# Optimization experiments

Measured on AMD Instinct MI355X. Metric: run time of the kernel, lower is better.

Reference implementation:

```python
import jax, jax.numpy as jnp
import numpy as np

N = 100000      # nodes
E = 1600000     # edges (avg degree 16)
IN = 64         # input feature dim
HID = 64        # hidden dim per head
HEADS = 4
OUT = 7         # hardcoded out_dim in GCNNet


def setup_inputs() -> dict:
    key = jax.random.key(0)
    ks = jax.random.split(key, 24)

    def p(k, shape, fan_in):
        return jax.random.normal(k, shape, jnp.float32) / jnp.float32(np.sqrt(fan_in))

    inp = {}
    inp["feature"] = jax.random.normal(ks[0], (N, IN), jnp.float32)
    inp["src"] = jax.random.randint(ks[1], (E,), 0, N, jnp.int32)
    inp["dst"] = jax.random.randint(ks[2], (E,), 0, N, jnp.int32)
    # layer 0: 4 heads (IN->HID) + head_linear GCN_Attention (4*HID->HID)
    inp["W0"] = p(ks[3], (HEADS, IN, HID), IN)
    inp["b0"] = jnp.zeros((HEADS, HID), jnp.float32)
    inp["a0"] = p(ks[4], (HEADS, 2 * HID), 2 * HID)
    inp["W0h"] = p(ks[5], (HEADS * HID, HID), HEADS * HID)
    inp["b0h"] = jnp.zeros((HID,), jnp.float32)
    inp["a0h"] = p(ks[6], (2 * HID,), 2 * HID)
    # layer 1: 4 heads (HID->HID) + head_linear (4*HID->HID)
    inp["W1"] = p(ks[7], (HEADS, HID, HID), HID)
    inp["b1"] = jnp.zeros((HEADS, HID), jnp.float32)
    inp["a1"] = p(ks[8], (HEADS, 2 * HID), 2 * HID)
    inp["W1h"] = p(ks[9], (HEADS * HID, HID), HEADS * HID)
    inp["b1h"] = jnp.zeros((HID,), jnp.float32)
    inp["a1h"] = p(ks[10], (2 * HID,), 2 * HID)
    # out layer: mean mode, 4 heads (HID->OUT) + Linear(OUT, OUT)
    inp["Wo"] = p(ks[11], (HEADS, HID, OUT), HID)
    inp["bo"] = jnp.zeros((HEADS, OUT), jnp.float32)
    inp["ao"] = p(ks[12], (HEADS, 2 * OUT), 2 * OUT)
    inp["lin_W"] = p(ks[13], (OUT, OUT), OUT)   # stored (in, out)
    inp["lin_b"] = jnp.zeros((OUT,), jnp.float32)
    return inp


def gcn_attn(feat, W, b, a, src, dst):
    """One GCN_Attention layer: edge score = GELU(attn_fc(cat(z_src, z_dst))),
    per-dst softmax over incoming edges, weighted sum of src z."""
    z = feat @ W + b                       # [N, d]
    d = z.shape[1]
    # attn_fc has no bias: attn(cat(s, t)) = s @ a[:d] + t @ a[d:]
    s_l = z @ a[:d]                        # [N]
    s_r = z @ a[d:]                        # [N]
    e = jax.nn.gelu(s_l[src] + s_r[dst], approximate=False)   # [E]
    # segmented softmax over incoming edges of each dst node
    m = jax.ops.segment_max(e, dst, num_segments=N)
    m = jnp.where(jnp.isfinite(m), m, 0.0)
    ex = jnp.exp(e - m[dst])
    denom = jax.ops.segment_sum(ex, dst, num_segments=N)
    alpha = ex / denom[dst]                # [E]
    h = jax.ops.segment_sum(alpha[:, None] * z[src], dst, num_segments=N)  # [N, d]
    return h


def reference(feature, src, dst, W0, b0, a0, W0h, b0h, a0h,
              W1, b1, a1, W1h, b1h, a1h, Wo, bo, ao, lin_W, lin_b):
    # layer 0 (concat mode)
    h0 = jnp.concatenate([gcn_attn(feature, W0[i], b0[i], a0[i], src, dst)
                          for i in range(HEADS)], axis=1)      # [N, 4*HID]
    f1 = gcn_attn(h0, W0h, b0h, a0h, src, dst)                 # [N, HID]
    # layer 1 (concat mode)
    h1 = jnp.concatenate([gcn_attn(f1, W1[i], b1[i], a1[i], src, dst)
                          for i in range(HEADS)], axis=1)
    f2 = gcn_attn(h1, W1h, b1h, a1h, src, dst)                 # [N, HID]
    # out layer (mean mode)
    outs = jnp.mean(jnp.stack([gcn_attn(f2, Wo[i], bo[i], ao[i], src, dst)
                               for i in range(HEADS)]), axis=0)  # [N, OUT]
    out = outs @ lin_W + lin_b
    return jax.nn.softmax(out, axis=1)
```

## Files before the change

### kernel.cpp

```cpp
#include <hip/hip_runtime.h>
#include <hip/hip_bf16.h>
#include <math.h>

#define HEADS 4
#define HID 64
#define OUTD 7

typedef __attribute__((ext_vector_type(8))) short bf16x8;
typedef __attribute__((ext_vector_type(4))) float f32x4;

__device__ __forceinline__ float gelu_exact(float x) {
    return 0.5f * x * (1.0f + erff(x * 0.70710678118654752f));
}

__device__ __forceinline__ float readlane_f(float v, int k) {
    union { float f; int i; } u;
    u.f = v;
    u.i = __builtin_amdgcn_readlane(u.i, k);
    return u.f;
}
__device__ __forceinline__ int readlane_i(int v, int k) {
    return __builtin_amdgcn_readlane(v, k);
}

__device__ __forceinline__ unsigned int f2bf(float f) {
    unsigned int x = __float_as_uint(f);
    return (x + 0x7fffu + ((x >> 16) & 1u)) >> 16;
}
__device__ __forceinline__ float bf_lo(unsigned int v) {
    return __uint_as_float(v << 16);
}
__device__ __forceinline__ float bf_hi(unsigned int v) {
    return __uint_as_float(v & 0xffff0000u);
}


__global__ void hist_kernel(const int* __restrict__ dst, int* __restrict__ cnt, int E) {
    for (int e = blockIdx.x * blockDim.x + threadIdx.x; e < E; e += gridDim.x * blockDim.x)
        atomicAdd(&cnt[dst[e]], 1);
}

__global__ __launch_bounds__(256) void scan1_kernel(const int* __restrict__ cnt,
                                                    int* __restrict__ rowptr,
                                                    int* __restrict__ bsum, int Nn) {
    __shared__ int sums[256];
    int t = threadIdx.x;
    int base = blockIdx.x * 2048 + t * 8;
    int orig[8];
    int run = 0;
#pragma unroll
    for (int i = 0; i < 8; i++) {
        orig[i] = (base + i < Nn) ? cnt[base + i] : 0;
        run += orig[i];
    }
    sums[t] = run;
    __syncthreads();
    for (int off = 1; off < 256; off <<= 1) {
        int y = (t >= off) ? sums[t - off] : 0;
        __syncthreads();
        sums[t] += y;
        __syncthreads();
    }
    int excl = sums[t] - run;
    if (t == 255) bsum[blockIdx.x] = sums[255];
    int e = excl;
#pragma unroll
    for (int i = 0; i < 8; i++) {
        if (base + i < Nn) rowptr[base + i] = e;
        e += orig[i];
    }
}

__global__ void scan2_kernel(int* __restrict__ bsum, int* __restrict__ rowptr, int nb, int Nn) {
    if (blockIdx.x == 0 && threadIdx.x == 0) {
        int run = 0;
        for (int i = 0; i < nb; i++) {
            int t = bsum[i];
            bsum[i] = run;
            run += t;
        }
        rowptr[Nn] = run;
    }
}

__global__ void scan3_kernel(int* __restrict__ rowptr, const int* __restrict__ bsum, int Nn) {
    int i = blockIdx.x * blockDim.x + threadIdx.x;
    if (i < Nn) rowptr[i] += bsum[i >> 11];
}

__global__ void scatter_kernel(const int* __restrict__ dst, const int* __restrict__ rowptr,
                               int* __restrict__ cnt, const int* __restrict__ srcv,
                               int* __restrict__ srcp, int E) {
    for (int e = blockIdx.x * blockDim.x + threadIdx.x; e < E; e += gridDim.x * blockDim.x) {
        int d = dst[e];
        int p = rowptr[d] + atomicAdd(&cnt[d], 1);
        srcp[p] = srcv[e];
    }
}

__global__ void wconv_kernel(const float* __restrict__ W, unsigned short* __restrict__ Wt) {
    int m = blockIdx.x, k = threadIdx.x;
    Wt[m * 256 + k] = (unsigned short)f2bf(W[k * 64 + m]);
}


template <int MODE>
__global__ __launch_bounds__(256, 2) void gemm_kernel(const float* __restrict__ X,
                                                      const float* __restrict__ Wt,
                                                      const float* __restrict__ Bt,
                                                      const float* __restrict__ Aw,
                                                      unsigned short* __restrict__ Zb,
                                                      float* __restrict__ Zf,
                                                      float* __restrict__ SLo,
                                                      float* __restrict__ SRo, int Nn) {
    constexpr int K = 64;
    constexpr int M = (MODE == 0) ? 256 : 32;
    constexpr int CPL = (MODE == 0) ? 4 : 1;

    __shared__ float wlds[K * M];

    const int tid = threadIdx.x;
    const int wid = tid >> 6;
    const int lane = tid & 63;
    const int row0 = blockIdx.x * 32 + wid * 8;

    if (MODE == 0) {
#pragma unroll
        for (int it = 0; it < 16; ++it) {
            int flat = it * 1024 + tid * 4;
            int k = flat >> 8, m = flat & 255;
            int h = m >> 6, c = m & 63;
            *(float4*)&wlds[flat] = *(const float4*)(Wt + h * 4096 + k * 64 + c);
        }
    } else {
#pragma unroll
        for (int it = 0; it < 8; ++it) {
            int idx = it * 256 + tid;
            int k = idx >> 5, m = idx & 31, h = m >> 3, j = m & 7;
            wlds[idx] = (j < 7) ? Wt[h * 448 + k * 7 + j] : 0.f;
        }
    }
    __syncthreads();

    float acc[8][CPL];
#pragma unroll
    for (int r = 0; r < 8; ++r)
#pragma unroll
        for (int c = 0; c < CPL; ++c) acc[r][c] = 0.f;

    float xr[8];
#pragma unroll
    for (int r = 0; r < 8; ++r) {
        int rr = row0 + r;
        rr = (rr < Nn) ? rr : (Nn - 1);
        xr[r] = X[(size_t)rr * 64 + lane];
    }
#pragma unroll 4
    for (int k = 0; k < 64; ++k) {
        if (MODE == 0) {
            float4 wv = *(const float4*)&wlds[k * 256 + lane * 4];
#pragma unroll
            for (int r = 0; r < 8; ++r) {
                float xk = readlane_f(xr[r], k);
                acc[r][0] = fmaf(xk, wv.x, acc[r][0]);
                acc[r][1] = fmaf(xk, wv.y, acc[r][1]);
                acc[r][2] = fmaf(xk, wv.z, acc[r][2]);
                acc[r][3] = fmaf(xk, wv.w, acc[r][3]);
            }
        } else {
            float wv = wlds[k * 32 + (lane & 31)];
#pragma unroll
            for (int r = 0; r < 8; ++r)
                acc[r][0] = fmaf(readlane_f(xr[r], k), wv, acc[r][0]);
        }
    }

    if (MODE == 0) {
        float4 bv = *(const float4*)(Bt + lane * 4);
        const int h = lane >> 4;
        const int c0 = (lane & 15) * 4;
        float4 al4 = *(const float4*)(Aw + h * 128 + c0);
        float4 ar4 = *(const float4*)(Aw + h * 128 + 64 + c0);
        const int t = lane;
        const int lsbase = t >> 2;
#pragma unroll
        for (int r = 0; r < 8; ++r) {
            int row = row0 + r;
            float4 s = {acc[r][0] + bv.x, acc[r][1] + bv.y, acc[r][2] + bv.z, acc[r][3] + bv.w};
            float sp = s.x * al4.x + s.y * al4.y + s.z * al4.z + s.w * al4.w;
            float rp = s.x * ar4.x + s.y * ar4.y + s.z * ar4.z + s.w * ar4.w;
#pragma unroll
            for (int o = 1; o < 16; o <<= 1) {
                sp += __shfl_xor(sp, o);
                rp += __shfl_xor(rp, o);
            }
            unsigned int lo = f2bf(s.x) | (f2bf(s.y) << 16);
            unsigned int hi = f2bf(s.z) | (f2bf(s.w) << 16);
            unsigned int us[4];
#pragma unroll
            for (int h2 = 0; h2 < 4; ++h2) {
                int ls = (h2 << 4) | lsbase;
                unsigned int vlo = (unsigned int)__shfl((int)lo, ls);
                unsigned int vhi = (unsigned int)__shfl((int)hi, ls);
                unsigned int v = (t & 2) ? vhi : vlo;
                us[h2] = (t & 1) ? (v >> 16) : (v & 0xffffu);
            }
            if (row < Nn) {
                uint2 pk = {us[0] | (us[1] << 16), us[2] | (us[3] << 16)};
                *(uint2*)(Zb + (size_t)row * 256 + t * 4) = pk;
                if ((lane & 15) == 0) {
                    SLo[(size_t)row * 4 + h] = sp;
                    SRo[(size_t)row * 4 + h] = rp;
                }
            }
        }
    } else {
        if (lane < 32) {
            int m = lane, h = m >> 3, j = m & 7;
            float bvv = (j < 7) ? Bt[h * 7 + j] : 0.f;
            float al = (j < 7) ? Aw[h * 14 + j] : 0.f;
            float ar = (j < 7) ? Aw[h * 14 + 7 + j] : 0.f;
#pragma unroll
            for (int r = 0; r < 8; ++r) {
                int row = row0 + r;
                float zv = (j < 7) ? acc[r][0] + bvv : 0.f;
                float sp = zv * al, rp = zv * ar;
#pragma unroll
                for (int o = 1; o < 8; o <<= 1) {
                    sp += __shfl_xor(sp, o);
                    rp += __shfl_xor(rp, o);
                }
                if (row < Nn) {
                    Zf[(size_t)row * 32 + m] = zv;
                    if (j == 0) {
                        SLo[(size_t)row * 4 + h] = sp;
                        SRo[(size_t)row * 4 + h] = rp;
                    }
                }
            }
        }
    }
}


__global__ __launch_bounds__(256) void gemm1_mfma_kernel(
    const unsigned short* __restrict__ X, const unsigned short* __restrict__ Wt,
    const float* __restrict__ Bt, const float* __restrict__ Aw,
    unsigned short* __restrict__ Zb, float* __restrict__ SLo, float* __restrict__ SRo,
    int Nn) {
    const int tid = threadIdx.x;
    const int wid = tid >> 6;
    const int lane = tid & 63;
    const int g = lane >> 4, i = lane & 15;
    const int rowbase = blockIdx.x * 64 + wid * 16;

    int arow = rowbase + i;
    if (arow >= Nn) arow = Nn - 1;
    const bf16x8* xa = (const bf16x8*)(X + (size_t)arow * 256 + g * 8);
    const bf16x8* w0 = (const bf16x8*)(Wt + (size_t)(i) * 256 + g * 8);
    const bf16x8* w1 = (const bf16x8*)(Wt + (size_t)(16 + i) * 256 + g * 8);
    const bf16x8* w2 = (const bf16x8*)(Wt + (size_t)(32 + i) * 256 + g * 8);
    const bf16x8* w3 = (const bf16x8*)(Wt + (size_t)(48 + i) * 256 + g * 8);

    f32x4 acc0 = {0.f, 0.f, 0.f, 0.f};
    f32x4 acc1 = acc0, acc2 = acc0, acc3 = acc0;
#pragma unroll
    for (int ks = 0; ks < 8; ++ks) {
        bf16x8 av = xa[ks * 4];
        bf16x8 b0 = w0[ks * 4];
        bf16x8 b1 = w1[ks * 4];
        bf16x8 b2 = w2[ks * 4];
        bf16x8 b3 = w3[ks * 4];
        acc0 = __builtin_amdgcn_mfma_f32_16x16x32_bf16(av, b0, acc0, 0, 0, 0);
        acc1 = __builtin_amdgcn_mfma_f32_16x16x32_bf16(av, b1, acc1, 0, 0, 0);
        acc2 = __builtin_amdgcn_mfma_f32_16x16x32_bf16(av, b2, acc2, 0, 0, 0);
        acc3 = __builtin_amdgcn_mfma_f32_16x16x32_bf16(av, b3, acc3, 0, 0, 0);
    }

    float bv0 = Bt[i], bv1 = Bt[16 + i], bv2 = Bt[32 + i], bv3 = Bt[48 + i];
    float al0 = Aw[i], al1 = Aw[16 + i], al2 = Aw[32 + i], al3 = Aw[48 + i];
    float ar0 = Aw[64 + i], ar1 = Aw[80 + i], ar2 = Aw[96 + i], ar3 = Aw[112 + i];
    float z0[4], z1[4], z2[4], z3[4], sp[4], rp[4];
#pragma unroll
    for (int r = 0; r < 4; ++r) {
        z0[r] = acc0[r] + bv0;
        z1[r] = acc1[r] + bv1;
        z2[r] = acc2[r] + bv2;
        z3[r] = acc3[r] + bv3;
        sp[r] = z0[r] * al0 + z1[r] * al1 + z2[r] * al2 + z3[r] * al3;
        rp[r] = z0[r] * ar0 + z1[r] * ar1 + z2[r] * ar2 + z3[r] * ar3;
    }
#pragma unroll
    for (int o = 1; o <= 8; o <<= 1) {
#pragma unroll
        for (int r = 0; r < 4; ++r) {
            sp[r] += __shfl_xor(sp[r], o);
            rp[r] += __shfl_xor(rp[r], o);
        }
    }
#pragma unroll
    for (int r = 0; r < 4; ++r) {
        int row = rowbase + g * 4 + r;
        if (row < Nn) {
            unsigned short* zp = Zb + (size_t)row * 64 + i;
            zp[0] = (unsigned short)f2bf(z0[r]);
            zp[16] = (unsigned short)f2bf(z1[r]);
            zp[32] = (unsigned short)f2bf(z2[r]);
            zp[48] = (unsigned short)f2bf(z3[r]);
            if (i == 0) {
                SLo[row] = sp[r];
                SRo[row] = rp[r];
            }
        }
    }
}


#define MAX4_REDUCE(m0, m1, m2, m3)                      \
    _Pragma("unroll") for (int off = 32; off; off >>= 1) { \
        m0 = fmaxf(m0, __shfl_xor(m0, off));             \
        m1 = fmaxf(m1, __shfl_xor(m1, off));             \
        m2 = fmaxf(m2, __shfl_xor(m2, off));             \
        m3 = fmaxf(m3, __shfl_xor(m3, off));             \
    }

#define SUM4_REDUCE(d0, d1, d2, d3)                      \
    _Pragma("unroll") for (int off = 32; off; off >>= 1) { \
        d0 += __shfl_xor(d0, off);                       \
        d1 += __shfl_xor(d1, off);                       \
        d2 += __shfl_xor(d2, off);                       \
        d3 += __shfl_xor(d3, off);                       \
    }

__global__ __launch_bounds__(256) void aggregate4_kernel(
    const unsigned short* __restrict__ Zb, const float* __restrict__ SL,
    const float* __restrict__ SR, const int* __restrict__ rowptr,
    const int* __restrict__ srcp, unsigned short* __restrict__ Hb, int Nn) {
    __shared__ int sstage[4][64];
    __shared__ float4 wstage[4][64];
    int wid = threadIdx.x >> 6;
    int n = (blockIdx.x * blockDim.x + threadIdx.x) >> 6;
    int lane = threadIdx.x & 63;
    if (n >= Nn) return;
    int s0 = rowptr[n], s1 = rowptr[n + 1];
    int deg = s1 - s0;
    unsigned short* hp = Hb + (size_t)n * 256 + lane;
    if (deg == 0) {
        hp[0] = 0; hp[64] = 0; hp[128] = 0; hp[192] = 0;
        return;
    }
    const float4 sr4 = *(const float4*)(SR + (size_t)n * 4);
    float hx = 0.f, hy = 0.f, hz = 0.f, hw = 0.f;
    float d0 = 0.f, d1 = 0.f, d2 = 0.f, d3 = 0.f;
    const unsigned laneoff = (unsigned)(lane * 8);

#define AGG4_EDGE_LDS(JJ)                                                    \
    {                                                                        \
        int s = sstage[wid][(JJ)];                                           \
        float4 w = wstage[wid][(JJ)];                                        \
        uint2 q = *(const uint2*)((const char*)Zb + ((unsigned)s * 512u + laneoff)); \
        hx = fmaf(w.x, bf_lo(q.x), hx);                                      \
        hy = fmaf(w.y, bf_hi(q.x), hy);                                      \
        hz = fmaf(w.z, bf_lo(q.y), hz);                                      \
        hw = fmaf(w.w, bf_hi(q.y), hw);                                      \
    }

    if (deg <= 64) {
        float e0 = -INFINITY, e1 = -INFINITY, e2 = -INFINITY, e3 = -INFINITY;
        int sv = 0;
        if (lane < deg) {
            sv = srcp[s0 + lane];
            float4 sl4 = *(const float4*)(SL + (size_t)sv * 4);
            e0 = gelu_exact(sl4.x + sr4.x);
            e1 = gelu_exact(sl4.y + sr4.y);
            e2 = gelu_exact(sl4.z + sr4.z);
            e3 = gelu_exact(sl4.w + sr4.w);
        }
        float m0 = e0, m1 = e1, m2 = e2, m3 = e3;
        MAX4_REDUCE(m0, m1, m2, m3)
        float ex0 = 0.f, ex1 = 0.f, ex2 = 0.f, ex3 = 0.f;
        if (lane < deg) {
            ex0 = __expf(e0 - m0); ex1 = __expf(e1 - m1);
            ex2 = __expf(e2 - m2); ex3 = __expf(e3 - m3);
        }
        d0 = ex0; d1 = ex1; d2 = ex2; d3 = ex3;
        if (lane < deg) {
            sstage[wid][lane] = sv;
            wstage[wid][lane] = make_float4(ex0, ex1, ex2, ex3);
        }
        int jj = 0;
        for (; jj + 3 < deg; jj += 4) {
            AGG4_EDGE_LDS(jj)
            AGG4_EDGE_LDS(jj + 1)
            AGG4_EDGE_LDS(jj + 2)
            AGG4_EDGE_LDS(jj + 3)
        }
        for (; jj < deg; ++jj) AGG4_EDGE_LDS(jj)
    } else {
        float m0 = -INFINITY, m1 = -INFINITY, m2 = -INFINITY, m3 = -INFINITY;
        for (int base = s0; base < s1; base += 64) {
            int j = base + lane;
            if (j < s1) {
                int s = srcp[j];
                float4 sl4 = *(const float4*)(SL + (size_t)s * 4);
                m0 = fmaxf(m0, gelu_exact(sl4.x + sr4.x));
                m1 = fmaxf(m1, gelu_exact(sl4.y + sr4.y));
                m2 = fmaxf(m2, gelu_exact(sl4.z + sr4.z));
                m3 = fmaxf(m3, gelu_exact(sl4.w + sr4.w));
            }
        }
        MAX4_REDUCE(m0, m1, m2, m3)
        for (int base = s0; base < s1; base += 64) {
            int j = base + lane;
            int sv = 0;
            float ex0 = 0.f, ex1 = 0.f, ex2 = 0.f, ex3 = 0.f;
            if (j < s1) {
                sv = srcp[j];
                float4 sl4 = *(const float4*)(SL + (size_t)sv * 4);
                ex0 = __expf(gelu_exact(sl4.x + sr4.x) - m0);
                ex1 = __expf(gelu_exact(sl4.y + sr4.y) - m1);
                ex2 = __expf(gelu_exact(sl4.z + sr4.z) - m2);
                ex3 = __expf(gelu_exact(sl4.w + sr4.w) - m3);
            }
            d0 += ex0; d1 += ex1; d2 += ex2; d3 += ex3;
            int cs = min(64, s1 - base);
            for (int jj = 0; jj < cs; ++jj) {
                int s = readlane_i(sv, jj);
                float a0 = readlane_f(ex0, jj), a1 = readlane_f(ex1, jj);
                float a2 = readlane_f(ex2, jj), a3 = readlane_f(ex3, jj);
                uint2 q = *(const uint2*)((const char*)Zb + ((unsigned)s * 512u + laneoff));
                hx = fmaf(a0, bf_lo(q.x), hx);
                hy = fmaf(a1, bf_hi(q.x), hy);
                hz = fmaf(a2, bf_lo(q.y), hz);
                hw = fmaf(a3, bf_hi(q.y), hw);
            }
        }
    }
#undef AGG4_EDGE_LDS
    SUM4_REDUCE(d0, d1, d2, d3)
    hp[0] = (unsigned short)f2bf(hx / d0);
    hp[64] = (unsigned short)f2bf(hy / d1);
    hp[128] = (unsigned short)f2bf(hz / d2);
    hp[192] = (unsigned short)f2bf(hw / d3);
}

__global__ __launch_bounds__(256) void aggregate1_kernel(
    const unsigned short* __restrict__ Zb, const float* __restrict__ SL,
    const float* __restrict__ SR, const int* __restrict__ rowptr,
    const int* __restrict__ srcp, float* __restrict__ Hout, int Nn) {
    __shared__ int s1s[4][64];
    __shared__ float w1s[4][64];
    int wid = threadIdx.x >> 6;
    int n = (blockIdx.x * blockDim.x + threadIdx.x) >> 6;
    int lane = threadIdx.x & 63;
    if (n >= Nn) return;
    int s0 = rowptr[n], s1 = rowptr[n + 1];
    int deg = s1 - s0;
    if (deg == 0) {
        Hout[(size_t)n * 64 + lane] = 0.f;
        return;
    }
    const float srn = SR[n];
    float hacc = 0.f, den = 0.f;
    const unsigned laneoff = (unsigned)(lane * 2);

    if (deg <= 64) {
        float e = -INFINITY;
        int sv = 0;
        if (lane < deg) {
            sv = srcp[s0 + lane];
            e = gelu_exact(SL[sv] + srn);
        }
        float m = e;
#pragma unroll
        for (int off = 32; off; off >>= 1) m = fmaxf(m, __shfl_xor(m, off));
        float ex = (lane < deg) ? __expf(e - m) : 0.f;
        den = ex;
        if (lane < deg) {
            s1s[wid][lane] = sv;
            w1s[wid][lane] = ex;
        }
        int jj = 0;
        for (; jj + 3 < deg; jj += 4) {
#pragma unroll
            for (int u = 0; u < 4; ++u) {
                int s = s1s[wid][jj + u];
                float b = w1s[wid][jj + u];
                unsigned short zq = *(const unsigned short*)((const char*)Zb +
                                                             ((unsigned)s * 128u + laneoff));
                hacc = fmaf(b, bf_lo((unsigned int)zq), hacc);
            }
        }
        for (; jj < deg; ++jj) {
            int s = s1s[wid][jj];
            float b = w1s[wid][jj];
            unsigned short zq = *(const unsigned short*)((const char*)Zb +
                                                         ((unsigned)s * 128u + laneoff));
            hacc = fmaf(b, bf_lo((unsigned int)zq), hacc);
        }
    } else {
        float m = -INFINITY;
        for (int base = s0; base < s1; base += 64) {
            int j = base + lane;
            if (j < s1) m = fmaxf(m, gelu_exact(SL[srcp[j]] + srn));
        }
#pragma unroll
        for (int off = 32; off; off >>= 1) m = fmaxf(m, __shfl_xor(m, off));
        for (int base = s0; base < s1; base += 64) {
            int j = base + lane;
            int sv = 0;
            float ex = 0.f;
            if (j < s1) {
                sv = srcp[j];
                ex = __expf(gelu_exact(SL[sv] + srn) - m);
            }
            den += ex;
            int cs = min(64, s1 - base);
            for (int jj = 0; jj < cs; ++jj) {
                int s = readlane_i(sv, jj);
                float b = readlane_f(ex, jj);
                hacc = fmaf(b, bf_lo((unsigned int)Zb[(size_t)s * 64 + lane]), hacc);
            }
        }
    }
#pragma unroll
    for (int off = 32; off; off >>= 1) den += __shfl_xor(den, off);
    Hout[(size_t)n * 64 + lane] = hacc / den;
}

__global__ __launch_bounds__(256) void aggregateo_kernel(
    const float* __restrict__ Z, const float* __restrict__ SL, const float* __restrict__ SR,
    const int* __restrict__ rowptr, const int* __restrict__ srcp,
    float* __restrict__ Hout, int Nn) {
    int n = (blockIdx.x * blockDim.x + threadIdx.x) >> 6;
    int lane = threadIdx.x & 63;
    if (n >= Nn) return;
    int s0 = rowptr[n], s1 = rowptr[n + 1];
    int deg = s1 - s0;
    if (deg == 0) {
        if (lane < 32) Hout[(size_t)n * 32 + lane] = 0.f;
        return;
    }
    const float4 sr4 = *(const float4*)(SR + (size_t)n * 4);
    const int h = (lane & 31) >> 3;
    const int eo = lane >> 5;
    float hacc = 0.f;
    float d0 = 0.f, d1 = 0.f, d2 = 0.f, d3 = 0.f;
    const float* zl = Z + (lane & 31);

    if (deg <= 64) {
        float e0 = -INFINITY, e1 = -INFINITY, e2 = -INFINITY, e3 = -INFINITY;
        int sv = 0;
        if (lane < deg) {
            sv = srcp[s0 + lane];
            float4 sl4 = *(const float4*)(SL + (size_t)sv * 4);
            e0 = gelu_exact(sl4.x + sr4.x);
            e1 = gelu_exact(sl4.y + sr4.y);
            e2 = gelu_exact(sl4.z + sr4.z);
            e3 = gelu_exact(sl4.w + sr4.w);
        }
        float m0 = e0, m1 = e1, m2 = e2, m3 = e3;
        MAX4_REDUCE(m0, m1, m2, m3)
        float ex0 = 0.f, ex1 = 0.f, ex2 = 0.f, ex3 = 0.f;
        if (lane < deg) {
            ex0 = __expf(e0 - m0); ex1 = __expf(e1 - m1);
            ex2 = __expf(e2 - m2); ex3 = __expf(e3 - m3);
        }
        d0 = ex0; d1 = ex1; d2 = ex2; d3 = ex3;
        for (int jj = 0; jj < deg; jj += 2) {
            int lsrc = jj + eo;
            int s = __shfl(sv, lsrc);
            float b0 = __shfl(ex0, lsrc), b1 = __shfl(ex1, lsrc);
            float b2 = __shfl(ex2, lsrc), b3 = __shfl(ex3, lsrc);
            float exs = (h == 0) ? b0 : (h == 1) ? b1 : (h == 2) ? b2 : b3;
            hacc = fmaf(exs, zl[(size_t)s * 32], hacc);
        }
    } else {
        float m0 = -INFINITY, m1 = -INFINITY, m2 = -INFINITY, m3 = -INFINITY;
        for (int base = s0; base < s1; base += 64) {
            int j = base + lane;
            if (j < s1) {
                int s = srcp[j];
                float4 sl4 = *(const float4*)(SL + (size_t)s * 4);
                m0 = fmaxf(m0, gelu_exact(sl4.x + sr4.x));
                m1 = fmaxf(m1, gelu_exact(sl4.y + sr4.y));
                m2 = fmaxf(m2, gelu_exact(sl4.z + sr4.z));
                m3 = fmaxf(m3, gelu_exact(sl4.w + sr4.w));
            }
        }
        MAX4_REDUCE(m0, m1, m2, m3)
        for (int base = s0; base < s1; base += 64) {
            int j = base + lane;
            int sv = 0;
            float ex0 = 0.f, ex1 = 0.f, ex2 = 0.f, ex3 = 0.f;
            if (j < s1) {
                sv = srcp[j];
                float4 sl4 = *(const float4*)(SL + (size_t)sv * 4);
                ex0 = __expf(gelu_exact(sl4.x + sr4.x) - m0);
                ex1 = __expf(gelu_exact(sl4.y + sr4.y) - m1);
                ex2 = __expf(gelu_exact(sl4.z + sr4.z) - m2);
                ex3 = __expf(gelu_exact(sl4.w + sr4.w) - m3);
            }
            d0 += ex0; d1 += ex1; d2 += ex2; d3 += ex3;
            int cs = min(64, s1 - base);
            for (int jj = 0; jj < cs; jj += 2) {
                int lsrc = jj + eo;
                int s = __shfl(sv, lsrc);
                float b0 = __shfl(ex0, lsrc), b1 = __shfl(ex1, lsrc);
                float b2 = __shfl(ex2, lsrc), b3 = __shfl(ex3, lsrc);
                float exs = (h == 0) ? b0 : (h == 1) ? b1 : (h == 2) ? b2 : b3;
                hacc = fmaf(exs, zl[(size_t)s * 32], hacc);
            }
        }
    }
    SUM4_REDUCE(d0, d1, d2, d3)
    hacc += __shfl_xor(hacc, 32);
    float dsel = (h == 0) ? d0 : (h == 1) ? d1 : (h == 2) ? d2 : d3;
    if (lane < 32) Hout[(size_t)n * 32 + lane] = hacc / dsel;
}


__global__ void finalize_kernel(const float* __restrict__ Hs, const float* __restrict__ LW,
                                const float* __restrict__ LB, float* __restrict__ out, int Nn) {
    int n = blockIdx.x * blockDim.x + threadIdx.x;
    if (n >= Nn) return;
    float mean[7];
#pragma unroll
    for (int k = 0; k < 7; k++)
        mean[k] = 0.25f * (Hs[(size_t)n * 32 + k] + Hs[(size_t)n * 32 + 8 + k] +
                           Hs[(size_t)n * 32 + 16 + k] + Hs[(size_t)n * 32 + 24 + k]);
    float lg[7];
#pragma unroll
    for (int o = 0; o < 7; o++) {
        float acc = LB[o];
#pragma unroll
        for (int k = 0; k < 7; k++) acc = fmaf(mean[k], LW[k * 7 + o], acc);
        lg[o] = acc;
    }
    float mx = lg[0];
#pragma unroll
    for (int o = 1; o < 7; o++) mx = fmaxf(mx, lg[o]);
    float s = 0.f;
#pragma unroll
    for (int o = 0; o < 7; o++) {
        lg[o] = __expf(lg[o] - mx);
        s += lg[o];
    }
    float inv = 1.f / s;
#pragma unroll
    for (int o = 0; o < 7; o++) out[(size_t)n * 7 + o] = lg[o] * inv;
}


extern "C" void kernel_launch(void* const* d_in, const int* in_sizes, int n_in,
                              void* d_out, int out_size, void* d_ws, size_t ws_size,
                              hipStream_t stream) {
    const float* feature = (const float*)d_in[0];
    const int* src = (const int*)d_in[1];
    const int* dst = (const int*)d_in[2];
    const float* W0 = (const float*)d_in[3];
    const float* b0 = (const float*)d_in[4];
    const float* a0 = (const float*)d_in[5];
    const float* W0h = (const float*)d_in[6];
    const float* b0h = (const float*)d_in[7];
    const float* a0h = (const float*)d_in[8];
    const float* W1 = (const float*)d_in[9];
    const float* b1 = (const float*)d_in[10];
    const float* a1 = (const float*)d_in[11];
    const float* W1h = (const float*)d_in[12];
    const float* b1h = (const float*)d_in[13];
    const float* a1h = (const float*)d_in[14];
    const float* Wo = (const float*)d_in[15];
    const float* bo = (const float*)d_in[16];
    const float* ao = (const float*)d_in[17];
    const float* linW = (const float*)d_in[18];
    const float* linb = (const float*)d_in[19];
    const int N = in_sizes[0] / 64;
    const int E = in_sizes[1];
    float* out = (float*)d_out;

    char* ws = (char*)d_ws;
    size_t off = 0;
    auto alloc = [&](size_t bytes) {
        void* p = ws + off;
        off += (bytes + 255) & ~(size_t)255;
        return p;
    };
    int* cnt = (int*)alloc((size_t)N * 4);
    int* rowptr = (int*)alloc(((size_t)N + 1) * 4);
    int* bsum = (int*)alloc(256 * 4);
    int* srcp = (int*)alloc((size_t)E * 4);
    unsigned short* zbf = (unsigned short*)alloc((size_t)N * 256 * 2);
    unsigned short* hbufb = (unsigned short*)alloc((size_t)N * 256 * 2);
    unsigned short* wtb = (unsigned short*)alloc(64 * 256 * 2);
    float* zo = (float*)alloc((size_t)N * 32 * 4);
    float* fbuf = (float*)alloc((size_t)N * 64 * 4);
    float* slb = (float*)alloc((size_t)N * 4 * 4);
    float* srb = (float*)alloc((size_t)N * 4 * 4);
    float* houts = fbuf;

    hipMemsetAsync(cnt, 0, (size_t)N * 4, stream);
    hist_kernel<<<2048, 256, 0, stream>>>(dst, cnt, E);
    int nb = (N + 2047) / 2048;
    scan1_kernel<<<nb, 256, 0, stream>>>(cnt, rowptr, bsum, N);
    scan2_kernel<<<1, 32, 0, stream>>>(bsum, rowptr, nb, N);
    scan3_kernel<<<(N + 255) / 256, 256, 0, stream>>>(rowptr, bsum, N);
    hipMemsetAsync(cnt, 0, (size_t)N * 4, stream);
    scatter_kernel<<<2048, 256, 0, stream>>>(dst, rowptr, cnt, src, srcp, E);

    int gemm_blocks = (N + 31) / 32;
    int mfma_blocks = (N + 63) / 64;
    int ablk = (N + 3) / 4;

    gemm_kernel<0><<<gemm_blocks, 256, 0, stream>>>(feature, W0, b0, a0, zbf, nullptr, slb, srb, N);
    aggregate4_kernel<<<ablk, 256, 0, stream>>>(zbf, slb, srb, rowptr, srcp, hbufb, N);
    wconv_kernel<<<64, 256, 0, stream>>>(W0h, wtb);
    gemm1_mfma_kernel<<<mfma_blocks, 256, 0, stream>>>(hbufb, wtb, b0h, a0h, zbf, slb, srb, N);
    aggregate1_kernel<<<ablk, 256, 0, stream>>>(zbf, slb, srb, rowptr, srcp, fbuf, N);
    gemm_kernel<0><<<gemm_blocks, 256, 0, stream>>>(fbuf, W1, b1, a1, zbf, nullptr, slb, srb, N);
    aggregate4_kernel<<<ablk, 256, 0, stream>>>(zbf, slb, srb, rowptr, srcp, hbufb, N);
    wconv_kernel<<<64, 256, 0, stream>>>(W1h, wtb);
    gemm1_mfma_kernel<<<mfma_blocks, 256, 0, stream>>>(hbufb, wtb, b1h, a1h, zbf, slb, srb, N);
    aggregate1_kernel<<<ablk, 256, 0, stream>>>(zbf, slb, srb, rowptr, srcp, fbuf, N);
    gemm_kernel<2><<<gemm_blocks, 256, 0, stream>>>(fbuf, Wo, bo, ao, nullptr, zo, slb, srb, N);
    aggregateo_kernel<<<ablk, 256, 0, stream>>>(zo, slb, srb, rowptr, srcp, houts, N);
    finalize_kernel<<<(N + 255) / 256, 256, 0, stream>>>(houts, linW, linb, out, N);
}
```

Measured before the change: 1.025 ms.

## Use bf16 MFMA for head projections, store hidden features as bf16, record scatter ranks

Replaces the scalar readlane-based FP32 GEMM for the 4-head projections with a bf16 MFMA kernel. This needs a feature-to-bf16 conversion kernel and a transposed bf16 weight conversion. aggregate1 now writes its output in bf16, which feeds both the next MFMA GEMM and the output-layer GEMM, halving that buffer's traffic. The CSR build records per-edge atomic ranks during the histogram so the scatter pass needs no second atomic pass or memset. The cost is extra bf16 rounding of inputs and intermediate features, plus an extra rank array of size E.

Result: faster. 900.9 us (-12.1%).

```diff
diff --git a/kernel.cpp b/kernel.cpp
--- a/kernel.cpp
+++ b/kernel.cpp
@@ -34,10 +34,10 @@
     return __uint_as_float(v & 0xffff0000u);
 }
 
-
-__global__ void hist_kernel(const int* __restrict__ dst, int* __restrict__ cnt, int E) {
+__global__ void histrank_kernel(const int* __restrict__ dst, int* __restrict__ cnt,
+                                int* __restrict__ rank, int E) {
     for (int e = blockIdx.x * blockDim.x + threadIdx.x; e < E; e += gridDim.x * blockDim.x)
-        atomicAdd(&cnt[dst[e]], 1);
+        rank[e] = atomicAdd(&cnt[dst[e]], 1);
 }
 
 __global__ __launch_bounds__(256) void scan1_kernel(const int* __restrict__ cnt,
@@ -88,155 +88,108 @@
     if (i < Nn) rowptr[i] += bsum[i >> 11];
 }
 
-__global__ void scatter_kernel(const int* __restrict__ dst, const int* __restrict__ rowptr,
-                               int* __restrict__ cnt, const int* __restrict__ srcv,
-                               int* __restrict__ srcp, int E) {
-    for (int e = blockIdx.x * blockDim.x + threadIdx.x; e < E; e += gridDim.x * blockDim.x) {
-        int d = dst[e];
-        int p = rowptr[d] + atomicAdd(&cnt[d], 1);
-        srcp[p] = srcv[e];
-    }
-}
-
-__global__ void wconv_kernel(const float* __restrict__ W, unsigned short* __restrict__ Wt) {
+__global__ void scatter2_kernel(const int* __restrict__ dst, const int* __restrict__ rank,
+                                const int* __restrict__ rowptr, const int* __restrict__ srcv,
+                                int* __restrict__ srcp, int E) {
+    for (int e = blockIdx.x * blockDim.x + threadIdx.x; e < E; e += gridDim.x * blockDim.x)
+        srcp[rowptr[dst[e]] + rank[e]] = srcv[e];
+}
+
+__global__ void xconv_kernel(const float* __restrict__ X, unsigned short* __restrict__ Xb,
+                             int total4) {
+    int idx = blockIdx.x * blockDim.x + threadIdx.x;
+    if (idx < total4) {
+        float4 v = ((const float4*)X)[idx];
+        ushort4 o = {(unsigned short)f2bf(v.x), (unsigned short)f2bf(v.y),
+                     (unsigned short)f2bf(v.z), (unsigned short)f2bf(v.w)};
+        ((ushort4*)Xb)[idx] = o;
+    }
+}
+
+__global__ void wconv1_kernel(const float* __restrict__ W, unsigned short* __restrict__ Wt) {
     int m = blockIdx.x, k = threadIdx.x;
     Wt[m * 256 + k] = (unsigned short)f2bf(W[k * 64 + m]);
 }
 
-
-template <int MODE>
-__global__ __launch_bounds__(256, 2) void gemm_kernel(const float* __restrict__ X,
-                                                      const float* __restrict__ Wt,
-                                                      const float* __restrict__ Bt,
-                                                      const float* __restrict__ Aw,
-                                                      unsigned short* __restrict__ Zb,
-                                                      float* __restrict__ Zf,
-                                                      float* __restrict__ SLo,
-                                                      float* __restrict__ SRo, int Nn) {
-    constexpr int K = 64;
-    constexpr int M = (MODE == 0) ? 256 : 32;
-    constexpr int CPL = (MODE == 0) ? 4 : 1;
-
-    __shared__ float wlds[K * M];
-
-    const int tid = threadIdx.x;
-    const int wid = tid >> 6;
-    const int lane = tid & 63;
-    const int row0 = blockIdx.x * 32 + wid * 8;
-
-    if (MODE == 0) {
-#pragma unroll
-        for (int it = 0; it < 16; ++it) {
-            int flat = it * 1024 + tid * 4;
-            int k = flat >> 8, m = flat & 255;
-            int h = m >> 6, c = m & 63;
-            *(float4*)&wlds[flat] = *(const float4*)(Wt + h * 4096 + k * 64 + c);
-        }
-    } else {
-#pragma unroll
-        for (int it = 0; it < 8; ++it) {
-            int idx = it * 256 + tid;
-            int k = idx >> 5, m = idx & 31, h = m >> 3, j = m & 7;
-            wlds[idx] = (j < 7) ? Wt[h * 448 + k * 7 + j] : 0.f;
-        }
-    }
-    __syncthreads();
-
-    float acc[8][CPL];
-#pragma unroll
-    for (int r = 0; r < 8; ++r)
-#pragma unroll
-        for (int c = 0; c < CPL; ++c) acc[r][c] = 0.f;
-
-    float xr[8];
-#pragma unroll
-    for (int r = 0; r < 8; ++r) {
-        int rr = row0 + r;
-        rr = (rr < Nn) ? rr : (Nn - 1);
-        xr[r] = X[(size_t)rr * 64 + lane];
-    }
-#pragma unroll 4
-    for (int k = 0; k < 64; ++k) {
-        if (MODE == 0) {
-            float4 wv = *(const float4*)&wlds[k * 256 + lane * 4];
-#pragma unroll
-            for (int r = 0; r < 8; ++r) {
-                float xk = readlane_f(xr[r], k);
-                acc[r][0] = fmaf(xk, wv.x, acc[r][0]);
-                acc[r][1] = fmaf(xk, wv.y, acc[r][1]);
-                acc[r][2] = fmaf(xk, wv.z, acc[r][2]);
-                acc[r][3] = fmaf(xk, wv.w, acc[r][3]);
-            }
-        } else {
-            float wv = wlds[k * 32 + (lane & 31)];
-#pragma unroll
-            for (int r = 0; r < 8; ++r)
-                acc[r][0] = fmaf(readlane_f(xr[r], k), wv, acc[r][0]);
-        }
-    }
-
-    if (MODE == 0) {
-        float4 bv = *(const float4*)(Bt + lane * 4);
-        const int h = lane >> 4;
-        const int c0 = (lane & 15) * 4;
-        float4 al4 = *(const float4*)(Aw + h * 128 + c0);
-        float4 ar4 = *(const float4*)(Aw + h * 128 + 64 + c0);
-        const int t = lane;
-        const int lsbase = t >> 2;
-#pragma unroll
-        for (int r = 0; r < 8; ++r) {
-            int row = row0 + r;
-            float4 s = {acc[r][0] + bv.x, acc[r][1] + bv.y, acc[r][2] + bv.z, acc[r][3] + bv.w};
-            float sp = s.x * al4.x + s.y * al4.y + s.z * al4.z + s.w * al4.w;
-            float rp = s.x * ar4.x + s.y * ar4.y + s.z * ar4.z + s.w * ar4.w;
-#pragma unroll
-            for (int o = 1; o < 16; o <<= 1) {
-                sp += __shfl_xor(sp, o);
-                rp += __shfl_xor(rp, o);
-            }
-            unsigned int lo = f2bf(s.x) | (f2bf(s.y) << 16);
-            unsigned int hi = f2bf(s.z) | (f2bf(s.w) << 16);
-            unsigned int us[4];
-#pragma unroll
-            for (int h2 = 0; h2 < 4; ++h2) {
-                int ls = (h2 << 4) | lsbase;
-                unsigned int vlo = (unsigned int)__shfl((int)lo, ls);
-                unsigned int vhi = (unsigned int)__shfl((int)hi, ls);
-                unsigned int v = (t & 2) ? vhi : vlo;
-                us[h2] = (t & 1) ? (v >> 16) : (v & 0xffffu);
-            }
-            if (row < Nn) {
-                uint2 pk = {us[0] | (us[1] << 16), us[2] | (us[3] << 16)};
-                *(uint2*)(Zb + (size_t)row * 256 + t * 4) = pk;
-                if ((lane & 15) == 0) {
-                    SLo[(size_t)row * 4 + h] = sp;
-                    SRo[(size_t)row * 4 + h] = rp;
-                }
-            }
-        }
-    } else {
-        if (lane < 32) {
-            int m = lane, h = m >> 3, j = m & 7;
-            float bvv = (j < 7) ? Bt[h * 7 + j] : 0.f;
-            float al = (j < 7) ? Aw[h * 14 + j] : 0.f;
-            float ar = (j < 7) ? Aw[h * 14 + 7 + j] : 0.f;
-#pragma unroll
-            for (int r = 0; r < 8; ++r) {
-                int row = row0 + r;
-                float zv = (j < 7) ? acc[r][0] + bvv : 0.f;
-                float sp = zv * al, rp = zv * ar;
-#pragma unroll
-                for (int o = 1; o < 8; o <<= 1) {
-                    sp += __shfl_xor(sp, o);
-                    rp += __shfl_xor(rp, o);
-                }
-                if (row < Nn) {
-                    Zf[(size_t)row * 32 + m] = zv;
-                    if (j == 0) {
-                        SLo[(size_t)row * 4 + h] = sp;
-                        SRo[(size_t)row * 4 + h] = rp;
-                    }
-                }
+__global__ void wconv0_kernel(const float* __restrict__ W, unsigned short* __restrict__ Wt) {
+    int m = blockIdx.x, k = threadIdx.x;
+    int h = m >> 6, c = m & 63;
+    Wt[m * 64 + k] = (unsigned short)f2bf(W[h * 4096 + k * 64 + c]);
+}
+
+
+__global__ __launch_bounds__(256) void gemm0_mfma_kernel(
+    const unsigned short* __restrict__ Xb, const unsigned short* __restrict__ Wt,
+    const float* __restrict__ Bt, const float* __restrict__ Aw,
+    unsigned short* __restrict__ Zb, float* __restrict__ SLo, float* __restrict__ SRo,
+    int Nn) {
+    const int wid = threadIdx.x >> 6;
+    const int lane = threadIdx.x & 63;
+    const int g = lane >> 4, i = lane & 15;
+    const int rowbase = blockIdx.x * 64 + wid * 16;
+    int arow = rowbase + i;
+    if (arow >= Nn) arow = Nn - 1;
+    const bf16x8* xa = (const bf16x8*)(Xb + (size_t)arow * 64 + g * 8);
+
+    f32x4 acc[16];
+#pragma unroll
+    for (int j = 0; j < 16; ++j) acc[j] = (f32x4){0.f, 0.f, 0.f, 0.f};
+#pragma unroll
+    for (int ks = 0; ks < 2; ++ks) {
+        bf16x8 av = xa[ks * 4];
+#pragma unroll
+        for (int j = 0; j < 16; ++j) {
+            bf16x8 bv = *(const bf16x8*)(Wt + (size_t)(16 * j + i) * 64 + ks * 32 + g * 8);
+            acc[j] = __builtin_amdgcn_mfma_f32_16x16x32_bf16(av, bv, acc[j], 0, 0, 0);
+        }
+    }
+    float bvv[4][4], alv[4][4], arv[4][4];
+#pragma unroll
+    for (int h = 0; h < 4; ++h)
+#pragma unroll
+        for (int jj = 0; jj < 4; ++jj) {
+            int c = 16 * jj + i;
+            bvv[h][jj] = Bt[64 * h + c];
+            alv[h][jj] = Aw[h * 128 + c];
+            arv[h][jj] = Aw[h * 128 + 64 + c];
+        }
+#pragma unroll
+    for (int r = 0; r < 4; ++r) {
+        int row = rowbase + g * 4 + r;
+        float z[4][4], sp[4], rp[4];
+#pragma unroll
+        for (int h = 0; h < 4; ++h) {
+            sp[h] = 0.f;
+            rp[h] = 0.f;
+        }
+#pragma unroll
+        for (int h = 0; h < 4; ++h)
+#pragma unroll
+            for (int jj = 0; jj < 4; ++jj) {
+                float zv = acc[4 * h + jj][r] + bvv[h][jj];
+                z[h][jj] = zv;
+                sp[h] = fmaf(zv, alv[h][jj], sp[h]);
+                rp[h] = fmaf(zv, arv[h][jj], rp[h]);
+            }
+#pragma unroll
+        for (int o = 1; o < 16; o <<= 1) {
+#pragma unroll
+            for (int h = 0; h < 4; ++h) {
+                sp[h] += __shfl_xor(sp[h], o);
+                rp[h] += __shfl_xor(rp[h], o);
+            }
+        }
+        if (row < Nn) {
+#pragma unroll
+            for (int jj = 0; jj < 4; ++jj) {
+                unsigned int lo = f2bf(z[0][jj]) | (f2bf(z[1][jj]) << 16);
+                unsigned int hi = f2bf(z[2][jj]) | (f2bf(z[3][jj]) << 16);
+                uint2 pk = {lo, hi};
+                *(uint2*)(Zb + (size_t)row * 256 + (16 * jj + i) * 4) = pk;
+            }
+            if (i == 0) {
+                *(float4*)(SLo + (size_t)row * 4) = make_float4(sp[0], sp[1], sp[2], sp[3]);
+                *(float4*)(SRo + (size_t)row * 4) = make_float4(rp[0], rp[1], rp[2], rp[3]);
             }
         }
     }
@@ -257,7 +210,7 @@
     int arow = rowbase + i;
     if (arow >= Nn) arow = Nn - 1;
     const bf16x8* xa = (const bf16x8*)(X + (size_t)arow * 256 + g * 8);
-    const bf16x8* w0 = (const bf16x8*)(Wt + (size_t)(i) * 256 + g * 8);
+    const bf16x8* w0 = (const bf16x8*)(Wt + (size_t)(i)*256 + g * 8);
     const bf16x8* w1 = (const bf16x8*)(Wt + (size_t)(16 + i) * 256 + g * 8);
     const bf16x8* w2 = (const bf16x8*)(Wt + (size_t)(32 + i) * 256 + g * 8);
     const bf16x8* w3 = (const bf16x8*)(Wt + (size_t)(48 + i) * 256 + g * 8);
@@ -310,6 +263,69 @@
             if (i == 0) {
                 SLo[row] = sp[r];
                 SRo[row] = rp[r];
+            }
+        }
+    }
+}
+
+
+__global__ __launch_bounds__(256, 2) void gemm2_kernel(const unsigned short* __restrict__ Xb,
+                                                       const float* __restrict__ Wt,
+                                                       const float* __restrict__ Bt,
+                                                       const float* __restrict__ Aw,
+                                                       float* __restrict__ Zf,
+                                                       float* __restrict__ SLo,
+                                                       float* __restrict__ SRo, int Nn) {
+    __shared__ float wlds[64 * 32];
+    const int tid = threadIdx.x;
+    const int wid = tid >> 6;
+    const int lane = tid & 63;
+    const int row0 = blockIdx.x * 32 + wid * 8;
+
+#pragma unroll
+    for (int it = 0; it < 8; ++it) {
+        int idx = it * 256 + tid;
+        int k = idx >> 5, m = idx & 31, h = m >> 3, j = m & 7;
+        wlds[idx] = (j < 7) ? Wt[h * 448 + k * 7 + j] : 0.f;
+    }
+    __syncthreads();
+
+    float acc[8] = {};
+    float xr[8];
+#pragma unroll
+    for (int r = 0; r < 8; ++r) {
+        int rr = row0 + r;
+        rr = (rr < Nn) ? rr : (Nn - 1);
+        xr[r] = bf_lo((unsigned int)Xb[(size_t)rr * 64 + lane]);
+    }
+#pragma unroll 4
+    for (int k = 0; k < 64; ++k) {
+        float wv = wlds[k * 32 + (lane & 31)];
+#pragma unroll
+        for (int r = 0; r < 8; ++r) acc[r] = fmaf(readlane_f(xr[r], k), wv, acc[r]);
+    }
+
+    if (lane < 32) {
+        int m = lane, h = m >> 3, j = m & 7;
+        float bvv = (j < 7) ? Bt[h * 7 + j] : 0.f;
+        float al = (j < 7) ? Aw[h * 14 + j] : 0.f;
+        float ar = (j < 7) ? Aw[h * 14 + 7 + j] : 0.f;
+#pragma unroll
+        for (int r = 0; r < 8; ++r) {
+            int row = row0 + r;
+            float zv = (j < 7) ? acc[r] + bvv : 0.f;
+            float sp = zv * al, rp = zv * ar;
+#pragma unroll
+            for (int o = 1; o < 8; o <<= 1) {
+                sp += __shfl_xor(sp, o);
+                rp += __shfl_xor(rp, o);
+            }
+            if (row < Nn) {
+                Zf[(size_t)row * 32 + m] = zv;
+                if (j == 0) {
+                    SLo[(size_t)row * 4 + h] = sp;
+                    SRo[(size_t)row * 4 + h] = rp;
+                }
             }
         }
     }
@@ -447,7 +463,7 @@
 __global__ __launch_bounds__(256) void aggregate1_kernel(
     const unsigned short* __restrict__ Zb, const float* __restrict__ SL,
     const float* __restrict__ SR, const int* __restrict__ rowptr,
-    const int* __restrict__ srcp, float* __restrict__ Hout, int Nn) {
+    const int* __restrict__ srcp, unsigned short* __restrict__ Hout, int Nn) {
     __shared__ int s1s[4][64];
     __shared__ float w1s[4][64];
     int wid = threadIdx.x >> 6;
@@ -457,7 +473,7 @@
     int s0 = rowptr[n], s1 = rowptr[n + 1];
     int deg = s1 - s0;
     if (deg == 0) {
-        Hout[(size_t)n * 64 + lane] = 0.f;
+        Hout[(size_t)n * 64 + lane] = 0;
         return;
     }
     const float srn = SR[n];
@@ -525,7 +541,7 @@
     }
 #pragma unroll
     for (int off = 32; off; off >>= 1) den += __shfl_xor(den, off);
-    Hout[(size_t)n * 64 + lane] = hacc / den;
+    Hout[(size_t)n * 64 + lane] = (unsigned short)f2bf(hacc / den);
 }
 
 __global__ __launch_bounds__(256) void aggregateo_kernel(
@@ -689,40 +705,44 @@
     int* cnt = (int*)alloc((size_t)N * 4);
     int* rowptr = (int*)alloc(((size_t)N + 1) * 4);
     int* bsum = (int*)alloc(256 * 4);
+    int* rank = (int*)alloc((size_t)E * 4);
     int* srcp = (int*)alloc((size_t)E * 4);
     unsigned short* zbf = (unsigned short*)alloc((size_t)N * 256 * 2);
     unsigned short* hbufb = (unsigned short*)alloc((size_t)N * 256 * 2);
-    unsigned short* wtb = (unsigned short*)alloc(64 * 256 * 2);
+    unsigned short* wtb = (unsigned short*)alloc(256 * 64 * 2);
+    unsigned short* xfeat = (unsigned short*)alloc((size_t)N * 64 * 2);
+    unsigned short* fb16 = (unsigned short*)alloc((size_t)N * 64 * 2);
     float* zo = (float*)alloc((size_t)N * 32 * 4);
-    float* fbuf = (float*)alloc((size_t)N * 64 * 4);
     float* slb = (float*)alloc((size_t)N * 4 * 4);
     float* srb = (float*)alloc((size_t)N * 4 * 4);
-    float* houts = fbuf;
+    float* houts = (float*)fb16;
 
     hipMemsetAsync(cnt, 0, (size_t)N * 4, stream);
-    hist_kernel<<<2048, 256, 0, stream>>>(dst, cnt, E);
+    histrank_kernel<<<2048, 256, 0, stream>>>(dst, cnt, rank, E);
     int nb = (N + 2047) / 2048;
     scan1_kernel<<<nb, 256, 0, stream>>>(cnt, rowptr, bsum, N);
     scan2_kernel<<<1, 32, 0, stream>>>(bsum, rowptr, nb, N);
     scan3_kernel<<<(N + 255) / 256, 256, 0, stream>>>(rowptr, bsum, N);
-    hipMemsetAsync(cnt, 0, (size_t)N * 4, stream);
-    scatter_kernel<<<2048, 256, 0, stream>>>(dst, rowptr, cnt, src, srcp, E);
-
-    int gemm_blocks = (N + 31) / 32;
+    scatter2_kernel<<<2048, 256, 0, stream>>>(dst, rank, rowptr, src, srcp, E);
+    xconv_kernel<<<(N * 64 / 4 + 255) / 256, 256, 0, stream>>>(feature, xfeat, N * 64 / 4);
+
     int mfma_blocks = (N + 63) / 64;
+    int g2_blocks = (N + 31) / 32;
     int ablk = (N + 3) / 4;
 
-    gemm_kernel<0><<<gemm_blocks, 256, 0, stream>>>(feature, W0, b0, a0, zbf, nullptr, slb, srb, N);
+    wconv0_kernel<<<256, 64, 0, stream>>>(W0, wtb);
+    gemm0_mfma_kernel<<<mfma_blocks, 256, 0, stream>>>(xfeat, wtb, b0, a0, zbf, slb, srb, N);
     aggregate4_kernel<<<ablk, 256, 0, stream>>>(zbf, slb, srb, rowptr, srcp, hbufb, N);
-    wconv_kernel<<<64, 256, 0, stream>>>(W0h, wtb);
+    wconv1_kernel<<<64, 256, 0, stream>>>(W0h, wtb);
     gemm1_mfma_kernel<<<mfma_blocks, 256, 0, stream>>>(hbufb, wtb, b0h, a0h, zbf, slb, srb, N);
-    aggregate1_kernel<<<ablk, 256, 0, stream>>>(zbf, slb, srb, rowptr, srcp, fbuf, N);
-    gemm_kernel<0><<<gemm_blocks, 256, 0, stream>>>(fbuf, W1, b1, a1, zbf, nullptr, slb, srb, N);
+    aggregate1_kernel<<<ablk, 256, 0, stream>>>(zbf, slb, srb, rowptr, srcp, fb16, N);
+    wconv0_kernel<<<256, 64, 0, stream>>>(W1, wtb);
+    gemm0_mfma_kernel<<<mfma_blocks, 256, 0, stream>>>(fb16, wtb, b1, a1, zbf, slb, srb, N);
     aggregate4_kernel<<<ablk, 256, 0, stream>>>(zbf, slb, srb, rowptr, srcp, hbufb, N);
-    wconv_kernel<<<64, 256, 0, stream>>>(W1h, wtb);
+    wconv1_kernel<<<64, 256, 0, stream>>>(W1h, wtb);
     gemm1_mfma_kernel<<<mfma_blocks, 256, 0, stream>>>(hbufb, wtb, b1h, a1h, zbf, slb, srb, N);
-    aggregate1_kernel<<<ablk, 256, 0, stream>>>(zbf, slb, srb, rowptr, srcp, fbuf, N);
-    gemm_kernel<2><<<gemm_blocks, 256, 0, stream>>>(fbuf, Wo, bo, ao, nullptr, zo, slb, srb, N);
+    aggregate1_kernel<<<ablk, 256, 0, stream>>>(zbf, slb, srb, rowptr, srcp, fb16, N);
+    gemm2_kernel<<<g2_blocks, 256, 0, stream>>>(fb16, Wo, bo, ao, zo, slb, srb, N);
     aggregateo_kernel<<<ablk, 256, 0, stream>>>(zo, slb, srb, rowptr, srcp, houts, N);
     finalize_kernel<<<(N + 255) / 256, 256, 0, stream>>>(houts, linW, linb, out, N);
 }
```
